# Kernel optimization log

Hardware: AMD Instinct MI355X
Metric: run time of the kernel (lower is better)

The kernel has to match this reference:

```python
import jax, jax.numpy as jnp
import numpy as np

B = 16        # graphs per batch
NPG = 4096    # nodes per graph
N = B * NPG
EPG = 32768   # edges per graph
E = B * EPG
F_NODE, F_EDGE, G, H, A = 8, 4, 16, 128, 10


def setup_inputs() -> dict:
    key = jax.random.key(0)
    ks = jax.random.split(key, 32)
    x = jax.random.normal(ks[0], (N, F_NODE), jnp.float32)
    # random intra-graph edges, offset into the batched node id space
    src = jax.random.randint(ks[1], (B, EPG), 0, NPG)
    dst = jax.random.randint(ks[2], (B, EPG), 0, NPG)
    off = (jnp.arange(B) * NPG)[:, None]
    edge_index = jnp.stack([(src + off).reshape(-1), (dst + off).reshape(-1)]).astype(jnp.int64)
    edge_attr = jax.random.normal(ks[3], (E, F_EDGE), jnp.float32)
    global_state = jax.random.normal(ks[4], (B, G), jnp.float32)
    current_pipe_nodes = jax.random.randint(ks[5], (B, 2), 0, NPG).astype(jnp.int64)

    def w(k, shape):
        fan_in = shape[0] if len(shape) > 1 else shape[0]
        return jax.random.normal(k, shape, jnp.float32) * (1.0 / np.sqrt(fan_in))

    return dict(
        x=x, edge_index=edge_index, edge_attr=edge_attr,
        global_state=global_state, current_pipe_nodes=current_pipe_nodes,
        W_l1=w(ks[6], (F_NODE, H)), W_r1=w(ks[7], (F_NODE, H)), W_e1=w(ks[8], (F_EDGE, H)),
        att1=w(ks[9], (H,)), b1=jnp.zeros((H,), jnp.float32),
        W_l2=w(ks[10], (H, H)), W_r2=w(ks[11], (H, H)), W_e2=w(ks[12], (F_EDGE, H)),
        att2=w(ks[13], (H,)), b2=jnp.zeros((H,), jnp.float32),
        W_c=w(ks[14], (H + 2 * H + G, 256)), b_c=jnp.zeros((256,), jnp.float32),
        W_a1=w(ks[15], (256, 128)), b_a1=jnp.zeros((128,), jnp.float32),
        W_a2=w(ks[16], (128, A)), b_a2=jnp.zeros((A,), jnp.float32),
        W_v1=w(ks[17], (256, 128)), b_v1=jnp.zeros((128,), jnp.float32),
        W_v2=w(ks[18], (128, 1)), b_v2=jnp.zeros((1,), jnp.float32),
    )


def add_self_loops(edge_index, edge_attr, n):
    # PyG default: add_self_loops=True, fill_value='mean' -> loop attr is the
    # mean of incoming edge_attr per node (zeros if none).
    dst = edge_index[1]
    deg = jax.ops.segment_sum(jnp.ones(dst.shape, jnp.float32), dst, num_segments=n)
    loop_attr = jax.ops.segment_sum(edge_attr, dst, num_segments=n) / jnp.maximum(deg, 1.0)[:, None]
    loops = jnp.tile(jnp.arange(n, dtype=edge_index.dtype)[None, :], (2, 1))
    ei = jnp.concatenate([edge_index, loops], axis=1)
    ea = jnp.concatenate([edge_attr, loop_attr], axis=0)
    return ei, ea


def gatv2(x, ei, ea, Wl, Wr, We, att, bias, n):
    # GATv2Conv (heads=1): score = att . leaky_relu(Wl x_j + Wr x_i + We e_ij)
    # message = alpha_ij * (Wl x_j); segment softmax over incoming edges of i.
    src, dst = ei[0], ei[1]
    xl = x @ Wl                                   # [N,H]
    xr = x @ Wr                                   # [N,H]
    m = xl[src] + xr[dst] + ea @ We               # [E,H]
    s = jax.nn.leaky_relu(m, 0.2) @ att           # [E]
    smax = jax.ops.segment_max(s, dst, num_segments=n)
    ealpha = jnp.exp(s - smax[dst])
    denom = jax.ops.segment_sum(ealpha, dst, num_segments=n)
    alpha = ealpha / denom[dst]
    out = jax.ops.segment_sum(alpha[:, None] * xl[src], dst, num_segments=n)
    return out + bias


def reference(x, edge_index, edge_attr, global_state, current_pipe_nodes,
              W_l1, W_r1, W_e1, att1, b1,
              W_l2, W_r2, W_e2, att2, b2,
              W_c, b_c, W_a1, b_a1, W_a2, b_a2, W_v1, b_v1, W_v2, b_v2):
    ei, ea = add_self_loops(edge_index, edge_attr, N)
    h = jax.nn.relu(gatv2(x, ei, ea, W_l1, W_r1, W_e1, att1, b1, N))
    h = gatv2(h, ei, ea, W_l2, W_r2, W_e2, att2, b2, N)
    # global_mean_pool: graphs are contiguous equal-size blocks
    graph_emb = h.reshape(B, NPG, H).mean(axis=1)                       # [B,H]
    abs_idx = current_pipe_nodes + (jnp.arange(B) * NPG)[:, None]       # [B,2]
    pipe_emb = h[abs_idx.reshape(-1)].reshape(B, 2 * H)                 # [B,2H]
    comb = jnp.concatenate([graph_emb, pipe_emb, global_state], axis=1)
    feat = jax.nn.relu(comb @ W_c + b_c)
    logits = jax.nn.relu(feat @ W_a1 + b_a1) @ W_a2 + b_a2              # [B,A]
    value = jax.nn.relu(feat @ W_v1 + b_v1) @ W_v2 + b_v2               # [B,1]
    return jnp.concatenate([logits, value], axis=1)                     # [B,A+1]
```

## Files before the change

### kernel.cpp

```cpp
#include <hip/hip_runtime.h>
#include <math.h>

#define NN   65536
#define NPG  4096
#define NB   16
#define NE   524288
#define EPG  32768
#define SB   8
#define NH   128
#define FN   8
#define FE   4
#define NG   16
#define NA   10
#define NFRAG 2048

typedef __attribute__((ext_vector_type(8))) short bf16x8;
typedef __attribute__((ext_vector_type(4))) float f32x4;

static __device__ __forceinline__ short bf16rne(float f) {
    unsigned u = __builtin_bit_cast(unsigned, f);
    u += 0x7FFFu + ((u >> 16) & 1u);
    return (short)(u >> 16);
}

__global__ void hist_lin1_kernel(const int* __restrict__ ei, int* __restrict__ subhist,
                                 const float* __restrict__ x,
                                 const float* __restrict__ Wl, const float* __restrict__ Wr,
                                 const float* __restrict__ Wl2, const float* __restrict__ Wr2,
                                 bf16x8* __restrict__ wbf,
                                 float* __restrict__ xl, float* __restrict__ xr) {
    int bid = blockIdx.x;
    if (bid < NB * SB) {
        __shared__ int hh[NPG];
        int g = bid >> 3, sb = bid & 7;
        int t = threadIdx.x;
        for (int i = t; i < NPG; i += 256) hh[i] = 0;
        __syncthreads();
        const int* dstp = ei + NE + g * EPG + sb * (EPG / SB);
        for (int i = t; i < EPG / SB; i += 256)
            atomicAdd(&hh[dstp[i] - g * NPG], 1);
        __syncthreads();
        int* out = subhist + (size_t)bid * NPG;
        for (int i = t; i < NPG; i += 256) out[i] = hh[i];
    } else if (bid < NB * SB + 2) {
        int sel = bid - NB * SB;
        const float* W = sel ? Wr2 : Wl2;
        int t = threadIdx.x;
#pragma unroll
        for (int q = 0; q < 8; ++q) {
            int f = t * 8 + q;
            int lane = f & 63;
            int kgct = f >> 6;
            int kg = kgct & 3, ct = kgct >> 2;
            int kbase = kg * 32 + (lane >> 4) * 8;
            int c = ct * 16 + (lane & 15);
            bf16x8 v;
#pragma unroll
            for (int j = 0; j < 8; ++j)
                v[j] = bf16rne(W[(kbase + j) * NH + c]);
            wbf[sel * NFRAG + f] = v;
        }
    } else {
        __shared__ float row[2][FN];
        int b2 = bid - NB * SB - 2;
        int sub = threadIdx.x >> 7;
        int k = threadIdx.x & 127;
        int n = b2 * 2 + sub;
        if (k < FN) row[sub][k] = x[n * FN + k];
        __syncthreads();
        float al = 0.f, ar = 0.f;
#pragma unroll
        for (int j = 0; j < FN; ++j) {
            float v = row[sub][j];
            al += v * Wl[j * NH + k];
            ar += v * Wr[j * NH + k];
        }
        xl[n * NH + k] = al;
        xr[n * NH + k] = ar;
    }
}

__global__ __launch_bounds__(1024) void csr_fill_kernel(
        const int* __restrict__ ei, const int* __restrict__ subhist,
        int* __restrict__ offs, int2* __restrict__ csr) {
    __shared__ int cur[NPG];
    __shared__ int psum[1024];
    int bid = blockIdx.x;
    int g = bid >> 3, sb = bid & 7;
    int t = threadIdx.x;
    int base4 = t * 4;
    int dpre[4], loc[4];
    int run = 0;
#pragma unroll
    for (int i = 0; i < 4; ++i) {
        int nl = base4 + i;
        int d = 0, pre = 0;
#pragma unroll
        for (int s = 0; s < SB; ++s) {
            int v = subhist[((size_t)(g * SB + s)) * NPG + nl];
            pre += (s < sb) ? v : 0;
            d += v;
        }
        dpre[i] = pre;
        loc[i] = run;
        run += d;
    }
    psum[t] = run;
    __syncthreads();
    for (int s = 1; s < 1024; s <<= 1) {
        int add = (t >= s) ? psum[t - s] : 0;
        __syncthreads();
        psum[t] += add;
        __syncthreads();
    }
    int prefix = (t == 0) ? 0 : psum[t - 1];
    int ebase = g * EPG;
#pragma unroll
    for (int i = 0; i < 4; ++i) {
        int nl = base4 + i;
        int off = ebase + prefix + loc[i];
        cur[nl] = off + dpre[i];
        if (sb == 0) offs[g * NPG + nl] = off;
    }
    if (sb == 0 && g == NB - 1 && t == 0) offs[NN] = NE;
    __syncthreads();
    int e0 = g * EPG + sb * (EPG / SB);
#pragma unroll
    for (int i = 0; i < (EPG / SB) / 1024; ++i) {
        int e = e0 + i * 1024 + t;
        int dst = ei[NE + e];
        int src = ei[e];
        int pos = atomicAdd(&cur[dst - g * NPG], 1);
        csr[pos] = make_int2(src, e);
    }
}

__global__ __launch_bounds__(256) void gat_gather_kernel(
        const float4* __restrict__ xl, const float4* __restrict__ xr,
        const float4* __restrict__ ea,
        const int2* __restrict__ csr, const int* __restrict__ offs,
        const float* __restrict__ We, const float* __restrict__ att,
        const float* __restrict__ bias,
        unsigned short* __restrict__ hbf_out,
        float4* __restrict__ lattr_w, const float4* __restrict__ lattr_r,
        float4* __restrict__ gpart, float4* __restrict__ pipe,
        const int* __restrict__ cpn, int do_relu) {
    __shared__ float4 red[8][32];
    int grp = threadIdx.x >> 5;
    int lane = threadIdx.x & 31;
    int bid = blockIdx.x;
    int xcd = bid & 7, slot = bid >> 3;
    int g = xcd + ((slot >> 9) << 3);
    int blk = slot & 511;
    int node = g * NPG + blk * 8 + grp;

    float4 xr4 = xr[node * 32 + lane];
    float4 att4 = ((const float4*)att)[lane];
    const float4* We4 = (const float4*)We;
    float4 we0 = We4[lane];
    float4 we1 = We4[32 + lane];
    float4 we2 = We4[64 + lane];
    float4 we3 = We4[96 + lane];

    int beg = offs[node], end = offs[node + 1];
    float l = 0.f;
    float4 acc = make_float4(0.f, 0.f, 0.f, 0.f);
    float4 easum = make_float4(0.f, 0.f, 0.f, 0.f);
    bool have_lattr = (lattr_r != nullptr);
    if (beg < end) {
        int last = end - 1;
        int2 se0 = csr[beg];
        int p1 = (beg + 1 <= last) ? beg + 1 : last;
        int2 se1 = csr[p1];
        float4 xl0 = xl[se0.x * 32 + lane];
        float4 a0 = ea[se0.y];
        for (int p = beg; p < end; ++p) {
            int p2 = (p + 2 <= last) ? p + 2 : last;
            int2 se2 = csr[p2];
            float4 xl1 = xl[se1.x * 32 + lane];
            float4 a1 = ea[se1.y];
            if (!have_lattr) {
                easum.x += a0.x; easum.y += a0.y; easum.z += a0.z; easum.w += a0.w;
            }
            float tx = xl0.x + xr4.x + a0.x * we0.x + a0.y * we1.x + a0.z * we2.x + a0.w * we3.x;
            float ty = xl0.y + xr4.y + a0.x * we0.y + a0.y * we1.y + a0.z * we2.y + a0.w * we3.y;
            float tz = xl0.z + xr4.z + a0.x * we0.z + a0.y * we1.z + a0.z * we2.z + a0.w * we3.z;
            float tw = xl0.w + xr4.w + a0.x * we0.w + a0.y * we1.w + a0.z * we2.w + a0.w * we3.w;
            tx = tx > 0.f ? tx : 0.2f * tx;
            ty = ty > 0.f ? ty : 0.2f * ty;
            tz = tz > 0.f ? tz : 0.2f * tz;
            tw = tw > 0.f ? tw : 0.2f * tw;
            float s = tx * att4.x + ty * att4.y + tz * att4.z + tw * att4.w;
#pragma unroll
            for (int o = 16; o >= 1; o >>= 1) s += __shfl_xor(s, o);
            float w = __expf(s);
            l += w;
            acc.x += w * xl0.x;
            acc.y += w * xl0.y;
            acc.z += w * xl0.z;
            acc.w += w * xl0.w;
            se1 = se2; xl0 = xl1; a0 = a1;
        }
    }
    {
        float ax, ay, az, aw;
        if (have_lattr) {
            float4 la = lattr_r[node];
            ax = la.x; ay = la.y; az = la.z; aw = la.w;
        } else {
            int deg = end - beg;
            float invd = 1.0f / (float)(deg > 0 ? deg : 1);
            ax = easum.x * invd; ay = easum.y * invd;
            az = easum.z * invd; aw = easum.w * invd;
            if (lane == 0) lattr_w[node] = make_float4(ax, ay, az, aw);
        }
        float4 xl4 = xl[node * 32 + lane];
        float tx = xl4.x + xr4.x + ax * we0.x + ay * we1.x + az * we2.x + aw * we3.x;
        float ty = xl4.y + xr4.y + ax * we0.y + ay * we1.y + az * we2.y + aw * we3.y;
        float tz = xl4.z + xr4.z + ax * we0.z + ay * we1.z + az * we2.z + aw * we3.z;
        float tw = xl4.w + xr4.w + ax * we0.w + ay * we1.w + az * we2.w + aw * we3.w;
        tx = tx > 0.f ? tx : 0.2f * tx;
        ty = ty > 0.f ? ty : 0.2f * ty;
        tz = tz > 0.f ? tz : 0.2f * tz;
        tw = tw > 0.f ? tw : 0.2f * tw;
        float s = tx * att4.x + ty * att4.y + tz * att4.z + tw * att4.w;
#pragma unroll
        for (int o = 16; o >= 1; o >>= 1) s += __shfl_xor(s, o);
        float w = __expf(s);
        l += w;
        acc.x += w * xl4.x;
        acc.y += w * xl4.y;
        acc.z += w * xl4.z;
        acc.w += w * xl4.w;
    }
    float inv = 1.0f / l;
    float4 b4 = ((const float4*)bias)[lane];
    float4 o4;
    o4.x = acc.x * inv + b4.x;
    o4.y = acc.y * inv + b4.y;
    o4.z = acc.z * inv + b4.z;
    o4.w = acc.w * inv + b4.w;
    if (do_relu) {
        o4.x = fmaxf(o4.x, 0.f); o4.y = fmaxf(o4.y, 0.f);
        o4.z = fmaxf(o4.z, 0.f); o4.w = fmaxf(o4.w, 0.f);
    }
    if (hbf_out != nullptr) {
        int rt = node >> 4, m = node & 15;
        int kg = lane >> 3, qd = (lane & 7) >> 1, j0 = (lane & 1) * 4;
        ushort4 v;
        v.x = (unsigned short)bf16rne(o4.x);
        v.y = (unsigned short)bf16rne(o4.y);
        v.z = (unsigned short)bf16rne(o4.z);
        v.w = (unsigned short)bf16rne(o4.w);
        *(ushort4*)&hbf_out[(size_t)(((rt * 4 + kg) * 64 + qd * 16 + m)) * 8 + j0] = v;
    } else {
        int nl = node - g * NPG;
        if (nl == cpn[g * 2 + 0]) pipe[(g * 2 + 0) * 32 + lane] = o4;
        if (nl == cpn[g * 2 + 1]) pipe[(g * 2 + 1) * 32 + lane] = o4;
    }

    if (gpart != nullptr) {
        red[grp][lane] = o4;
        __syncthreads();
        if (grp < 4) {
            float4 o = red[grp + 4][lane];
            red[grp][lane] = make_float4(red[grp][lane].x + o.x, red[grp][lane].y + o.y,
                                         red[grp][lane].z + o.z, red[grp][lane].w + o.w);
        }
        __syncthreads();
        if (grp < 2) {
            float4 o = red[grp + 2][lane];
            red[grp][lane] = make_float4(red[grp][lane].x + o.x, red[grp][lane].y + o.y,
                                         red[grp][lane].z + o.z, red[grp][lane].w + o.w);
        }
        __syncthreads();
        if (grp == 0) {
            float4 a = red[0][lane], b = red[1][lane];
            gpart[(g * 512 + blk) * 32 + lane] =
                make_float4(a.x + b.x, a.y + b.y, a.z + b.z, a.w + b.w);
        }
    }
}

__global__ __launch_bounds__(256) void lin2_mfma_kernel(
        const bf16x8* __restrict__ hbf, const bf16x8* __restrict__ wbf,
        float* __restrict__ xl, float* __restrict__ xr) {
    const bf16x8* Bf = wbf + (size_t)blockIdx.y * NFRAG;
    float* C = blockIdx.y ? xr : xl;
    int t = threadIdx.x;
    int wv = t >> 6, lane = t & 63;
    int rt = blockIdx.x * 4 + wv;
    int row0 = rt * 16;
    int m = lane & 15, qd = lane >> 4;
    bf16x8 afrag[4];
#pragma unroll
    for (int kg = 0; kg < 4; ++kg)
        afrag[kg] = hbf[(size_t)(rt * 4 + kg) * 64 + lane];
#pragma unroll
    for (int ct = 0; ct < 8; ++ct) {
        f32x4 acc = {0.f, 0.f, 0.f, 0.f};
#pragma unroll
        for (int kg = 0; kg < 4; ++kg) {
            bf16x8 b = Bf[((ct << 2) | kg) * 64 + lane];
            acc = __builtin_amdgcn_mfma_f32_16x16x32_bf16(afrag[kg], b, acc, 0, 0, 0);
        }
        int col = ct * 16 + m;
#pragma unroll
        for (int r = 0; r < 4; ++r)
            C[(size_t)(row0 + qd * 4 + r) * NH + col] = acc[r];
    }
}

__global__ __launch_bounds__(1024) void head_kernel(
        const float* __restrict__ gpart, const float* __restrict__ pipe,
        const float* __restrict__ gstate,
        const float* __restrict__ Wc, const float* __restrict__ bc,
        const float* __restrict__ Wa1, const float* __restrict__ ba1,
        const float* __restrict__ Wa2, const float* __restrict__ ba2,
        const float* __restrict__ Wv1, const float* __restrict__ bv1,
        const float* __restrict__ Wv2, const float* __restrict__ bv2,
        float* __restrict__ out) {
    int b = blockIdx.x, t = threadIdx.x;
    __shared__ float comb[400];
    __shared__ float part[4][256];
    __shared__ float pp[8][128];
    __shared__ float feat[256];
    __shared__ float hid[256];
    {
        int d = t & 127, p = t >> 7;
        const float* gp = gpart + (size_t)b * 512 * NH + d;
        float s = 0.f;
        int c0 = p * 64;
        for (int c = c0; c < c0 + 64; ++c) s += gp[c * NH];
        pp[p][d] = s;
    }
    if (t >= 128 && t < 384) comb[t] = pipe[(size_t)b * 2 * NH + (t - 128)];
    else if (t >= 384 && t < 400) comb[t] = gstate[b * NG + (t - 384)];
    __syncthreads();
    if (t < 128) {
        float s = pp[0][t] + pp[1][t] + pp[2][t] + pp[3][t]
                + pp[4][t] + pp[5][t] + pp[6][t] + pp[7][t];
        comb[t] = s * (1.0f / NPG);
    }
    __syncthreads();
    {
        int col = t & 255, p = t >> 8;
        float a = 0.f;
        int j0 = p * 100;
        for (int j = j0; j < j0 + 100; ++j) a += comb[j] * Wc[j * 256 + col];
        part[p][col] = a;
    }
    __syncthreads();
    if (t < 256)
        feat[t] = fmaxf(bc[t] + part[0][t] + part[1][t] + part[2][t] + part[3][t], 0.f);
    __syncthreads();
    {
        int col = t & 255, p = t >> 8;
        const float* W = (col < 128) ? Wa1 : Wv1;
        int cc = col & 127;
        float a = 0.f;
        int j0 = p * 64;
        for (int j = j0; j < j0 + 64; ++j) a += feat[j] * W[j * 128 + cc];
        part[p][col] = a;
    }
    __syncthreads();
    if (t < 256) {
        float bias = (t < 128) ? ba1[t] : bv1[t - 128];
        hid[t] = fmaxf(bias + part[0][t] + part[1][t] + part[2][t] + part[3][t], 0.f);
    }
    __syncthreads();
    if (t < NA) {
        float a2 = ba2[t];
        for (int j = 0; j < NH; ++j) a2 += hid[j] * Wa2[j * NA + t];
        out[b * 11 + t] = a2;
    } else if (t == NA) {
        float a2 = bv2[0];
        for (int j = 0; j < NH; ++j) a2 += hid[128 + j] * Wv2[j];
        out[b * 11 + 10] = a2;
    }
}

extern "C" void kernel_launch(void* const* d_in, const int* in_sizes, int n_in,
                              void* d_out, int out_size, void* d_ws, size_t ws_size,
                              hipStream_t stream) {
    const float* x      = (const float*)d_in[0];
    const int*   ei     = (const int*)d_in[1];
    const float* ea     = (const float*)d_in[2];
    const float* gstate = (const float*)d_in[3];
    const int*   cpn    = (const int*)d_in[4];
    const float* Wl1 = (const float*)d_in[5];
    const float* Wr1 = (const float*)d_in[6];
    const float* We1 = (const float*)d_in[7];
    const float* att1= (const float*)d_in[8];
    const float* b1  = (const float*)d_in[9];
    const float* Wl2 = (const float*)d_in[10];
    const float* Wr2 = (const float*)d_in[11];
    const float* We2 = (const float*)d_in[12];
    const float* att2= (const float*)d_in[13];
    const float* b2  = (const float*)d_in[14];
    const float* Wc  = (const float*)d_in[15];
    const float* bc  = (const float*)d_in[16];
    const float* Wa1 = (const float*)d_in[17];
    const float* ba1 = (const float*)d_in[18];
    const float* Wa2 = (const float*)d_in[19];
    const float* ba2 = (const float*)d_in[20];
    const float* Wv1 = (const float*)d_in[21];
    const float* bv1 = (const float*)d_in[22];
    const float* Wv2 = (const float*)d_in[23];
    const float* bv2 = (const float*)d_in[24];

    char* ws = (char*)d_ws;
    size_t o = 0;
    float* xl     = (float*)(ws + o); o += (size_t)NN * NH * 4;
    float* xr     = (float*)(ws + o); o += (size_t)NN * NH * 4;
    unsigned short* hbf = (unsigned short*)(ws + o); o += (size_t)NN * NH * 2;
    float* lattr  = (float*)(ws + o); o += (size_t)NN * 16;
    float* gpart  = (float*)(ws + o); o += (size_t)NB * 512 * NH * 4;
    float* pipe   = (float*)(ws + o); o += (size_t)NB * 2 * NH * 4;
    int*   offs   = (int*)(ws + o);   o += (((size_t)(NN + 1) * 4 + 255) & ~(size_t)255);
    int*   subhist= (int*)(ws + o);   o += (size_t)NB * SB * NPG * 4;
    int2*  csr    = (int2*)(ws + o);  o += (size_t)NE * 8;
    bf16x8* wbf   = (bf16x8*)(ws + o); o += (size_t)2 * NFRAG * 16;
    (void)o; (void)ws_size; (void)in_sizes; (void)n_in; (void)out_size;

    hist_lin1_kernel<<<NB * SB + 2 + NN / 2, 256, 0, stream>>>(ei, subhist, x, Wl1, Wr1,
                                                               Wl2, Wr2, wbf, xl, xr);
    csr_fill_kernel<<<NB * SB, 1024, 0, stream>>>(ei, subhist, offs, csr);
    gat_gather_kernel<<<NN / 8, 256, 0, stream>>>((const float4*)xl, (const float4*)xr,
        (const float4*)ea, csr, offs, We1, att1, b1, hbf,
        (float4*)lattr, nullptr, nullptr, nullptr, cpn, 1);
    lin2_mfma_kernel<<<dim3(NN / 64, 2), 256, 0, stream>>>((const bf16x8*)hbf, wbf, xl, xr);
    gat_gather_kernel<<<NN / 8, 256, 0, stream>>>((const float4*)xl, (const float4*)xr,
        (const float4*)ea, csr, offs, We2, att2, b2, nullptr,
        nullptr, (const float4*)lattr, (float4*)gpart, (float4*)pipe, cpn, 0);
    head_kernel<<<NB, 1024, 0, stream>>>(gpart, pipe, gstate, Wc, bc, Wa1, ba1, Wa2, ba2,
                                         Wv1, bv1, Wv2, bv2, (float*)d_out);
}
```

Baseline: 292.0 us.

## Move lin1 projection into CSR fill kernel and shrink histogram launch

The layer-1 linear projection moves out of the histogram kernel and into the CSR fill kernel as 512 extra blocks, so it runs alongside the serial-scan CSR blocks instead of inflating the histogram launch. The lin1 path now keeps weights in registers, uses vectorized x loads and processes 16 nodes per thread, replacing the earlier 32768 tiny blocks. The histogram kernel drops to 130 blocks of 1024 threads. The aim is to fill idle CUs during the latency-bound CSR scan and to cut block launch overhead. The cost is a mixed kernel with large shared memory on every block, which may limit occupancy for the lin1 blocks.

```diff
diff --git a/kernel.cpp b/kernel.cpp
--- a/kernel.cpp
+++ b/kernel.cpp
@@ -13,6 +13,7 @@
 #define NG   16
 #define NA   10
 #define NFRAG 2048
+#define L1B  512
 
 typedef __attribute__((ext_vector_type(8))) short bf16x8;
 typedef __attribute__((ext_vector_type(4))) float f32x4;
@@ -23,32 +24,29 @@
     return (short)(u >> 16);
 }
 
-__global__ void hist_lin1_kernel(const int* __restrict__ ei, int* __restrict__ subhist,
-                                 const float* __restrict__ x,
-                                 const float* __restrict__ Wl, const float* __restrict__ Wr,
-                                 const float* __restrict__ Wl2, const float* __restrict__ Wr2,
-                                 bf16x8* __restrict__ wbf,
-                                 float* __restrict__ xl, float* __restrict__ xr) {
+__global__ __launch_bounds__(1024) void hist_kernel(
+        const int* __restrict__ ei, int* __restrict__ subhist,
+        const float* __restrict__ Wl2, const float* __restrict__ Wr2,
+        bf16x8* __restrict__ wbf) {
     int bid = blockIdx.x;
+    int t = threadIdx.x;
     if (bid < NB * SB) {
         __shared__ int hh[NPG];
         int g = bid >> 3, sb = bid & 7;
-        int t = threadIdx.x;
-        for (int i = t; i < NPG; i += 256) hh[i] = 0;
+        for (int i = t; i < NPG; i += 1024) hh[i] = 0;
         __syncthreads();
         const int* dstp = ei + NE + g * EPG + sb * (EPG / SB);
-        for (int i = t; i < EPG / SB; i += 256)
+        for (int i = t; i < EPG / SB; i += 1024)
             atomicAdd(&hh[dstp[i] - g * NPG], 1);
         __syncthreads();
         int* out = subhist + (size_t)bid * NPG;
-        for (int i = t; i < NPG; i += 256) out[i] = hh[i];
-    } else if (bid < NB * SB + 2) {
+        for (int i = t; i < NPG; i += 1024) out[i] = hh[i];
+    } else {
         int sel = bid - NB * SB;
         const float* W = sel ? Wr2 : Wl2;
-        int t = threadIdx.x;
-#pragma unroll
-        for (int q = 0; q < 8; ++q) {
-            int f = t * 8 + q;
+#pragma unroll
+        for (int q = 0; q < 2; ++q) {
+            int f = t * 2 + q;
             int lane = f & 63;
             int kgct = f >> 6;
             int kg = kgct & 3, ct = kgct >> 2;
@@ -60,78 +58,88 @@
                 v[j] = bf16rne(W[(kbase + j) * NH + c]);
             wbf[sel * NFRAG + f] = v;
         }
+    }
+}
+
+__global__ __launch_bounds__(1024) void csr_lin1_kernel(
+        const int* __restrict__ ei, const int* __restrict__ subhist,
+        int* __restrict__ offs, int2* __restrict__ csr,
+        const float* __restrict__ x,
+        const float* __restrict__ Wl, const float* __restrict__ Wr,
+        float* __restrict__ xl, float* __restrict__ xr) {
+    int bid = blockIdx.x;
+    int t = threadIdx.x;
+    if (bid < NB * SB) {
+        __shared__ int cur[NPG];
+        __shared__ int psum[1024];
+        int g = bid >> 3, sb = bid & 7;
+        int base4 = t * 4;
+        int dpre[4], loc[4];
+        int run = 0;
+#pragma unroll
+        for (int i = 0; i < 4; ++i) {
+            int nl = base4 + i;
+            int d = 0, pre = 0;
+#pragma unroll
+            for (int s = 0; s < SB; ++s) {
+                int v = subhist[((size_t)(g * SB + s)) * NPG + nl];
+                pre += (s < sb) ? v : 0;
+                d += v;
+            }
+            dpre[i] = pre;
+            loc[i] = run;
+            run += d;
+        }
+        psum[t] = run;
+        __syncthreads();
+        for (int s = 1; s < 1024; s <<= 1) {
+            int add = (t >= s) ? psum[t - s] : 0;
+            __syncthreads();
+            psum[t] += add;
+            __syncthreads();
+        }
+        int prefix = (t == 0) ? 0 : psum[t - 1];
+        int ebase = g * EPG;
+#pragma unroll
+        for (int i = 0; i < 4; ++i) {
+            int nl = base4 + i;
+            int off = ebase + prefix + loc[i];
+            cur[nl] = off + dpre[i];
+            if (sb == 0) offs[g * NPG + nl] = off;
+        }
+        if (sb == 0 && g == NB - 1 && t == 0) offs[NN] = NE;
+        __syncthreads();
+        int e0 = g * EPG + sb * (EPG / SB);
+#pragma unroll
+        for (int i = 0; i < (EPG / SB) / 1024; ++i) {
+            int e = e0 + i * 1024 + t;
+            int dst = ei[NE + e];
+            int src = ei[e];
+            int pos = atomicAdd(&cur[dst - g * NPG], 1);
+            csr[pos] = make_int2(src, e);
+        }
     } else {
-        __shared__ float row[2][FN];
-        int b2 = bid - NB * SB - 2;
-        int sub = threadIdx.x >> 7;
-        int k = threadIdx.x & 127;
-        int n = b2 * 2 + sub;
-        if (k < FN) row[sub][k] = x[n * FN + k];
-        __syncthreads();
-        float al = 0.f, ar = 0.f;
+        int lb = bid - NB * SB;
+        int k = t & 127;
+        int oct = t >> 7;
+        float wl[FN], wr[FN];
 #pragma unroll
         for (int j = 0; j < FN; ++j) {
-            float v = row[sub][j];
-            al += v * Wl[j * NH + k];
-            ar += v * Wr[j * NH + k];
-        }
-        xl[n * NH + k] = al;
-        xr[n * NH + k] = ar;
-    }
-}
-
-__global__ __launch_bounds__(1024) void csr_fill_kernel(
-        const int* __restrict__ ei, const int* __restrict__ subhist,
-        int* __restrict__ offs, int2* __restrict__ csr) {
-    __shared__ int cur[NPG];
-    __shared__ int psum[1024];
-    int bid = blockIdx.x;
-    int g = bid >> 3, sb = bid & 7;
-    int t = threadIdx.x;
-    int base4 = t * 4;
-    int dpre[4], loc[4];
-    int run = 0;
-#pragma unroll
-    for (int i = 0; i < 4; ++i) {
-        int nl = base4 + i;
-        int d = 0, pre = 0;
-#pragma unroll
-        for (int s = 0; s < SB; ++s) {
-            int v = subhist[((size_t)(g * SB + s)) * NPG + nl];
-            pre += (s < sb) ? v : 0;
-            d += v;
-        }
-        dpre[i] = pre;
-        loc[i] = run;
-        run += d;
-    }
-    psum[t] = run;
-    __syncthreads();
-    for (int s = 1; s < 1024; s <<= 1) {
-        int add = (t >= s) ? psum[t - s] : 0;
-        __syncthreads();
-        psum[t] += add;
-        __syncthreads();
-    }
-    int prefix = (t == 0) ? 0 : psum[t - 1];
-    int ebase = g * EPG;
-#pragma unroll
-    for (int i = 0; i < 4; ++i) {
-        int nl = base4 + i;
-        int off = ebase + prefix + loc[i];
-        cur[nl] = off + dpre[i];
-        if (sb == 0) offs[g * NPG + nl] = off;
-    }
-    if (sb == 0 && g == NB - 1 && t == 0) offs[NN] = NE;
-    __syncthreads();
-    int e0 = g * EPG + sb * (EPG / SB);
-#pragma unroll
-    for (int i = 0; i < (EPG / SB) / 1024; ++i) {
-        int e = e0 + i * 1024 + t;
-        int dst = ei[NE + e];
-        int src = ei[e];
-        int pos = atomicAdd(&cur[dst - g * NPG], 1);
-        csr[pos] = make_int2(src, e);
+            wl[j] = Wl[j * NH + k];
+            wr[j] = Wr[j * NH + k];
+        }
+        int nbase = lb * 128 + oct * 16;
+        for (int i = 0; i < 16; ++i) {
+            int n = nbase + i;
+            float4 xa = *(const float4*)&x[(size_t)n * FN];
+            float4 xb = *(const float4*)&x[(size_t)n * FN + 4];
+            float al = xa.x * wl[0] + xa.y * wl[1] + xa.z * wl[2] + xa.w * wl[3]
+                     + xb.x * wl[4] + xb.y * wl[5] + xb.z * wl[6] + xb.w * wl[7];
+            float ar = xa.x * wr[0] + xa.y * wr[1] + xa.z * wr[2] + xa.w * wr[3]
+                     + xb.x * wr[4] + xb.y * wr[5] + xb.z * wr[6] + xb.w * wr[7];
+            xl[(size_t)n * NH + k] = al;
+            xr[(size_t)n * NH + k] = ar;
+        }
     }
 }
 
@@ -423,9 +431,9 @@
     bf16x8* wbf   = (bf16x8*)(ws + o); o += (size_t)2 * NFRAG * 16;
     (void)o; (void)ws_size; (void)in_sizes; (void)n_in; (void)out_size;
 
-    hist_lin1_kernel<<<NB * SB + 2 + NN / 2, 256, 0, stream>>>(ei, subhist, x, Wl1, Wr1,
-                                                               Wl2, Wr2, wbf, xl, xr);
-    csr_fill_kernel<<<NB * SB, 1024, 0, stream>>>(ei, subhist, offs, csr);
+    hist_kernel<<<NB * SB + 2, 1024, 0, stream>>>(ei, subhist, Wl2, Wr2, wbf);
+    csr_lin1_kernel<<<NB * SB + L1B, 1024, 0, stream>>>(ei, subhist, offs, csr,
+                                                        x, Wl1, Wr1, xl, xr);
     gat_gather_kernel<<<NN / 8, 256, 0, stream>>>((const float4*)xl, (const float4*)xr,
         (const float4*)ea, csr, offs, We1, att1, b1, hbf,
         (float4*)lattr, nullptr, nullptr, nullptr, cpn, 1);
```

After: 270.2 us. -7.5%, faster.
